# Kernel tuning notes

Measured on AMD Instinct MI355X. Metric: run time of the kernel, lower is better.

## Reference

```python
import jax, jax.numpy as jnp
import numpy as np

N = 8000      # nodes (spatial spots)
E = 40000     # directed edges (kNN graph, avg degree 5)
DIN = 1024    # input_dim
H = 3         # heads
C = 1024      # hidden_dim per head
NCLS = 460    # n_classes
NCEN = 100    # centroid count (pass-through only)
NEG_SLOPE = 0.2


def setup_inputs() -> dict:
    key = jax.random.key(0)
    ks = jax.random.split(key, 12)
    s_in = 1.0 / np.sqrt(DIN)   # glorot-ish scale for 1024 fan-in
    s_h = 1.0 / np.sqrt(C)
    return {
        'x': jax.random.normal(ks[0], (N, DIN), jnp.float32),
        'edge_index': jax.random.randint(ks[1], (E, 2), 0, N),  # [E,2] (src,dst)
        'Wl': jax.random.normal(ks[2], (DIN, H * C), jnp.float32) * s_in,
        'bl': jnp.zeros((H * C,), jnp.float32),
        'Wr': jax.random.normal(ks[3], (DIN, H * C), jnp.float32) * s_in,
        'br': jnp.zeros((H * C,), jnp.float32),
        'att': jax.random.normal(ks[4], (H, C), jnp.float32) * s_h,
        'bias': jnp.zeros((C,), jnp.float32),
        'Wf': jax.random.normal(ks[5], (C, NCLS), jnp.float32) * s_h,
        'bf': jnp.zeros((NCLS,), jnp.float32),
        'exps': jax.random.uniform(ks[6], (N, NCLS), jnp.float32),
        'exps_c': jax.random.uniform(ks[7], (NCEN, NCLS), jnp.float32),
    }


def reference(x, edge_index, Wl, bl, Wr, br, att, bias, Wf, bf, exps, exps_c):
    n = x.shape[0]
    h_, c_ = att.shape
    # PyG GATv2Conv default add_self_loops=True
    loops = jnp.arange(n)
    src = jnp.concatenate([edge_index[:, 0], loops])
    dst = jnp.concatenate([edge_index[:, 1], loops])
    # lin_l / lin_r projections -> [N,H,C]
    xl = (x @ Wl + bl).reshape(n, h_, c_)
    xr = (x @ Wr + br).reshape(n, h_, c_)
    # GATv2 edge scores: a^T LeakyReLU(x_l[src] + x_r[dst])  -> [Etot,H]
    s = jax.nn.leaky_relu(xl[src] + xr[dst], NEG_SLOPE)
    e = jnp.einsum('ehc,hc->eh', s, att)
    # segment softmax over incoming edges per dst node (PyG softmax: +1e-16)
    m = jax.lax.stop_gradient(jax.ops.segment_max(e, dst, num_segments=n))
    a = jnp.exp(e - m[dst])
    denom = jax.ops.segment_sum(a, dst, num_segments=n)
    alpha = a / (denom[dst] + 1e-16)
    # weighted scatter-add of source messages
    out = jax.ops.segment_sum(alpha[:, :, None] * xl[src], dst, num_segments=n)
    # concat=False -> mean over heads, then conv bias
    out = out.mean(axis=1) + bias
    # fc + row softmax
    h = jax.nn.softmax(out @ Wf + bf, axis=-1)
    return h
```

## Files before the change

kernel.cpp:

```cpp
#include <hip/hip_runtime.h>

#define NNODES 8000
#define MPAD   8064
#define NEDGES 40000
#define ETOT   (NEDGES + NNODES)
#define DIN    1024
#define NH     3
#define CH     1024
#define HC     (NH * CH)
#define NTOT   (2 * HC)
#define NCLS   460
#define NCLS_P 512
#define NEG    0.2f

typedef _Float16 h8 __attribute__((ext_vector_type(8)));
typedef _Float16 h4v __attribute__((ext_vector_type(4)));
typedef float    f4 __attribute__((ext_vector_type(4)));

__global__ __launch_bounds__(256)
void fp16_pad_convert(const float* __restrict__ in, _Float16* __restrict__ out,
                      int rows_in, int rows_out, int cols)
{
    size_t i4 = (size_t)blockIdx.x * 256 + threadIdx.x;
    size_t tot = ((size_t)rows_out * cols) >> 2;
    if (i4 >= tot) return;
    size_t e = i4 << 2;
    int row = (int)(e / cols);
    float vx = 0.f, vy = 0.f, vz = 0.f, vw = 0.f;
    if (row < rows_in) {
        float4 v = *(const float4*)(in + e);
        vx = v.x; vy = v.y; vz = v.z; vw = v.w;
    }
    h4v o = { (_Float16)vx, (_Float16)vy, (_Float16)vz, (_Float16)vw };
    *(h4v*)(out + e) = o;
}

__global__ __launch_bounds__(256)
void transpose_to_fp16(const float* __restrict__ W, _Float16* __restrict__ Wt,
                       int K, int Ncols, int rowOff)
{
    __shared__ float tile[32][33];
    int n0 = blockIdx.x * 32, k0 = blockIdx.y * 32;
    int tx = threadIdx.x, ty = threadIdx.y;
    #pragma unroll
    for (int i = 0; i < 4; ++i) {
        int k = k0 + ty + i * 8;
        int n = n0 + tx;
        tile[ty + i * 8][tx] = (n < Ncols) ? W[(size_t)k * Ncols + n] : 0.f;
    }
    __syncthreads();
    #pragma unroll
    for (int i = 0; i < 4; ++i) {
        int n = n0 + ty + i * 8;
        int k = k0 + tx;
        Wt[(size_t)(rowOff + n) * K + k] = (_Float16)tile[tx][ty + i * 8];
    }
}

__global__ __launch_bounds__(256)
void bias_pack(const float* __restrict__ bl, const float* __restrict__ br,
               const float* __restrict__ bf, float* __restrict__ b1, float* __restrict__ b2)
{
    int i = blockIdx.x * 256 + threadIdx.x;
    if (i < HC) { b1[i] = bl[i]; b1[HC + i] = br[i]; }
    if (i < NCLS_P) b2[i] = (i < NCLS) ? bf[i] : 0.f;
}

__global__ __launch_bounds__(256)
void csr_count(const int* __restrict__ ei, int* __restrict__ cnt)
{
    int e = blockIdx.x * 256 + threadIdx.x;
    if (e >= ETOT) return;
    int dst = (e < NEDGES) ? ei[2 * e + 1] : (e - NEDGES);
    atomicAdd(&cnt[dst], 1);
}

__global__ __launch_bounds__(1024)
void csr_scan(const int* __restrict__ cnt, int* __restrict__ rofs)
{
    __shared__ int s[1024];
    int t = threadIdx.x;
    int base = t * 8;
    int local[8];
    int sum = 0;
    #pragma unroll
    for (int i = 0; i < 8; ++i) {
        local[i] = sum;
        sum += (base + i < NNODES) ? cnt[base + i] : 0;
    }
    s[t] = sum;
    __syncthreads();
    for (int off = 1; off < 1024; off <<= 1) {
        int v = (t >= off) ? s[t - off] : 0;
        __syncthreads();
        if (t >= off) s[t] += v;
        __syncthreads();
    }
    int pre = (t > 0) ? s[t - 1] : 0;
    #pragma unroll
    for (int i = 0; i < 8; ++i)
        if (base + i < NNODES) rofs[base + i] = pre + local[i];
}

__global__ __launch_bounds__(256)
void csr_fill(const int* __restrict__ ei, const int* __restrict__ rofs,
              int* __restrict__ cursor, int* __restrict__ csr_src)
{
    int e = blockIdx.x * 256 + threadIdx.x;
    if (e >= ETOT) return;
    int src, dst;
    if (e < NEDGES) { src = ei[2 * e]; dst = ei[2 * e + 1]; }
    else            { src = dst = e - NEDGES; }
    int pos = rofs[dst] + atomicAdd(&cursor[dst], 1);
    csr_src[pos] = src;
}

__global__ __launch_bounds__(256, 3)
void gemm_f16(const _Float16* __restrict__ A, const _Float16* __restrict__ Bt,
              const float* __restrict__ biasN,
              float* __restrict__ C32, _Float16* __restrict__ C16,
              int N, int K)
{
    __shared__ __align__(16) _Float16 sA[128 * 32];
    __shared__ __align__(16) _Float16 sB[128 * 32];

    int nwg = gridDim.x;
    int orig = blockIdx.x;
    int q = nwg >> 3, r = nwg & 7;
    int xcd = orig & 7, idx = orig >> 3;
    int wg = (xcd < r ? xcd * (q + 1) : r * (q + 1) + (xcd - r) * q) + idx;
    int nbx = N >> 7;
    int bm = wg / nbx, bn = wg - bm * nbx;
    int m0 = bm << 7, n0 = bn << 7;

    const int t = threadIdx.x;
    const int lane = t & 63, w = t >> 6;
    const int wr = (w >> 1) << 6, wc = (w & 1) << 6;

    f4 acc[4][4];
    f4 zero = { 0.f, 0.f, 0.f, 0.f };
    #pragma unroll
    for (int i = 0; i < 4; ++i)
        #pragma unroll
        for (int j = 0; j < 4; ++j) acc[i][j] = zero;

    const int r0 = t >> 2, ks0 = t & 3;
    const int r1 = r0 + 64;
    const int wA0 = r0 * 32 + ((ks0 ^ ((r0 >> 1) & 3)) << 3);
    const int wA1 = r1 * 32 + ((ks0 ^ ((r1 >> 1) & 3)) << 3);
    const _Float16* gA0 = A  + (size_t)(m0 + r0) * K + ks0 * 8;
    const _Float16* gA1 = A  + (size_t)(m0 + r1) * K + ks0 * 8;
    const _Float16* gB0 = Bt + (size_t)(n0 + r0) * K + ks0 * 8;
    const _Float16* gB1 = Bt + (size_t)(n0 + r1) * K + ks0 * 8;

    uint4 stA0 = *(const uint4*)gA0;
    uint4 stA1 = *(const uint4*)gA1;
    uint4 stB0 = *(const uint4*)gB0;
    uint4 stB1 = *(const uint4*)gB1;

    const int nk = K >> 5;
    for (int s = 0; s < nk; ++s) {
        __syncthreads();
        *(uint4*)&sA[wA0] = stA0;
        *(uint4*)&sA[wA1] = stA1;
        *(uint4*)&sB[wA0] = stB0;
        *(uint4*)&sB[wA1] = stB1;
        __syncthreads();
        if (s + 1 < nk) {
            int koff = (s + 1) << 5;
            stA0 = *(const uint4*)(gA0 + koff);
            stA1 = *(const uint4*)(gA1 + koff);
            stB0 = *(const uint4*)(gB0 + koff);
            stB1 = *(const uint4*)(gB1 + koff);
        }
        const int ks = lane >> 4;
        h8 bh[4];
        #pragma unroll
        for (int nj = 0; nj < 4; ++nj) {
            int rn = wc + nj * 16 + (lane & 15);
            bh[nj] = *(const h8*)&sB[rn * 32 + ((ks ^ ((rn >> 1) & 3)) << 3)];
        }
        #pragma unroll
        for (int mi = 0; mi < 4; ++mi) {
            int rm = wr + mi * 16 + (lane & 15);
            h8 ah = *(const h8*)&sA[rm * 32 + ((ks ^ ((rm >> 1) & 3)) << 3)];
            #pragma unroll
            for (int nj = 0; nj < 4; ++nj)
                acc[mi][nj] = __builtin_amdgcn_mfma_f32_16x16x32_f16(ah, bh[nj], acc[mi][nj], 0, 0, 0);
        }
    }

    #pragma unroll
    for (int mi = 0; mi < 4; ++mi) {
        #pragma unroll
        for (int nj = 0; nj < 4; ++nj) {
            int col  = n0 + wc + nj * 16 + (lane & 15);
            int rowb = m0 + wr + mi * 16 + ((lane >> 4) << 2);
            float b = biasN[col];
            #pragma unroll
            for (int rg = 0; rg < 4; ++rg) {
                float v = acc[mi][nj][rg] + b;
                size_t off = (size_t)(rowb + rg) * N + col;
                if (C32) C32[off] = v;
                else     C16[off] = (_Float16)v;
            }
        }
    }
}

__global__ __launch_bounds__(384)
void edge_fused(const _Float16* __restrict__ xlr, const int* __restrict__ rofs,
                const int* __restrict__ cnt, const int* __restrict__ csr_src,
                const float* __restrict__ att, const float* __restrict__ bias,
                _Float16* __restrict__ o2h)
{
    __shared__ float red[6];
    __shared__ float outs[HC];

    const int dst = blockIdx.x;
    const int t   = threadIdx.x;
    const int h   = t >> 7;
    const int c0  = (t & 127) << 3;
    const int wid = t >> 6;

    h8 xrv = *(const h8*)(xlr + (size_t)dst * NTOT + HC + h * CH + c0);
    float xrf[8], atf[8];
    {
        float4 a0 = *(const float4*)(att + h * CH + c0);
        float4 a1 = *(const float4*)(att + h * CH + c0 + 4);
        atf[0] = a0.x; atf[1] = a0.y; atf[2] = a0.z; atf[3] = a0.w;
        atf[4] = a1.x; atf[5] = a1.y; atf[6] = a1.z; atf[7] = a1.w;
        #pragma unroll
        for (int j = 0; j < 8; ++j) xrf[j] = (float)xrv[j];
    }

    const int beg = rofs[dst];
    const int num = cnt[dst];

    float m = -3.4e38f, d = 0.f;
    float acc[8];
    #pragma unroll
    for (int j = 0; j < 8; ++j) acc[j] = 0.f;

    for (int i = 0; i < num; ++i) {
        int src = csr_src[beg + i];
        h8 xv = *(const h8*)(xlr + (size_t)src * NTOT + h * CH + c0);
        float s = 0.f;
        #pragma unroll
        for (int j = 0; j < 8; ++j) {
            float z = (float)xv[j] + xrf[j];
            z = z > 0.f ? z : NEG * z;
            s = fmaf(atf[j], z, s);
        }
        #pragma unroll
        for (int off = 32; off > 0; off >>= 1) s += __shfl_down(s, off);
        if ((t & 63) == 0) red[wid] = s;
        __syncthreads();
        float e = red[h << 1] + red[(h << 1) + 1];
        float nm = fmaxf(m, e);
        float sc_ = __expf(m - nm);
        float w   = __expf(e - nm);
        d = d * sc_ + w;
        #pragma unroll
        for (int j = 0; j < 8; ++j) acc[j] = fmaf(w, (float)xv[j], acc[j] * sc_);
        m = nm;
        __syncthreads();
    }

    float inv = 1.f / (d + 1e-16f) * (1.f / 3.f);
    #pragma unroll
    for (int j = 0; j < 8; ++j) outs[h * CH + c0 + j] = acc[j] * inv;
    __syncthreads();

    if (t < 256) {
        int c = t << 2;
        float4 b = *(const float4*)(bias + c);
        float v0 = outs[c + 0] + outs[CH + c + 0] + outs[2 * CH + c + 0] + b.x;
        float v1 = outs[c + 1] + outs[CH + c + 1] + outs[2 * CH + c + 1] + b.y;
        float v2 = outs[c + 2] + outs[CH + c + 2] + outs[2 * CH + c + 2] + b.z;
        float v3 = outs[c + 3] + outs[CH + c + 3] + outs[2 * CH + c + 3] + b.w;
        h4v o = { (_Float16)v0, (_Float16)v1, (_Float16)v2, (_Float16)v3 };
        *(h4v*)(o2h + (size_t)dst * CH + c) = o;
    }
}

__global__ __launch_bounds__(64)
void row_softmax(const float* __restrict__ logits, float* __restrict__ out)
{
    const int r = blockIdx.x;
    const int lane = threadIdx.x;
    const float* row = logits + (size_t)r * NCLS_P;
    float v[8];
    float mx = -3.4e38f;
    #pragma unroll
    for (int i = 0; i < 8; ++i) {
        int c = lane + i * 64;
        v[i] = (c < NCLS) ? row[c] : -3.4e38f;
        mx = fmaxf(mx, v[i]);
    }
    #pragma unroll
    for (int off = 32; off > 0; off >>= 1) mx = fmaxf(mx, __shfl_xor(mx, off));
    float s = 0.f;
    #pragma unroll
    for (int i = 0; i < 8; ++i) {
        int c = lane + i * 64;
        float ev = (c < NCLS) ? expf(v[i] - mx) : 0.f;
        v[i] = ev;
        s += ev;
    }
    #pragma unroll
    for (int off = 32; off > 0; off >>= 1) s += __shfl_xor(s, off);
    float inv = 1.f / s;
    #pragma unroll
    for (int i = 0; i < 8; ++i) {
        int c = lane + i * 64;
        if (c < NCLS) out[(size_t)r * NCLS + c] = v[i] * inv;
    }
}

extern "C" void kernel_launch(void* const* d_in, const int* in_sizes, int n_in,
                              void* d_out, int out_size, void* d_ws, size_t ws_size,
                              hipStream_t stream)
{
    (void)in_sizes; (void)n_in; (void)out_size; (void)ws_size;

    const float* x    = (const float*)d_in[0];
    const int*   ei   = (const int*)  d_in[1];
    const float* Wl   = (const float*)d_in[2];
    const float* bl   = (const float*)d_in[3];
    const float* Wr   = (const float*)d_in[4];
    const float* br   = (const float*)d_in[5];
    const float* att  = (const float*)d_in[6];
    const float* bias = (const float*)d_in[7];
    const float* Wf   = (const float*)d_in[8];
    const float* bf   = (const float*)d_in[9];

    char* base = (char*)d_ws;
    _Float16* xh      = (_Float16*)(base);
    _Float16* BtW     = (_Float16*)(base + 16515072);
    _Float16* Wft     = (_Float16*)(base + 29097984);
    float*    biasC1  = (float*)   (base + 30146560);
    float*    biasC2  = (float*)   (base + 30171136);
    int*      cnt     = (int*)     (base + 30173184);
    int*      cursor  = (int*)     (base + 30205184);
    int*      rofs    = (int*)     (base + 30237184);
    int*      csr_src = (int*)     (base + 30269184);
    _Float16* o2h     = (_Float16*)(base + 30461184);
    float*    logits  = (float*)   (base + 46976256);
    _Float16* xlr     = (_Float16*)(base + 63491328);

    hipMemsetAsync(cnt, 0, 64000, stream);
    hipMemsetAsync(o2h + (size_t)NNODES * CH, 0, (size_t)(MPAD - NNODES) * CH * 2, stream);

    fp16_pad_convert<<<(MPAD * DIN / 4 + 255) / 256, 256, 0, stream>>>(
        x, xh, NNODES, MPAD, DIN);

    transpose_to_fp16<<<dim3(HC / 32, DIN / 32), dim3(32, 8), 0, stream>>>(Wl, BtW, DIN, HC, 0);
    transpose_to_fp16<<<dim3(HC / 32, DIN / 32), dim3(32, 8), 0, stream>>>(Wr, BtW, DIN, HC, HC);
    transpose_to_fp16<<<dim3(NCLS_P / 32, DIN / 32), dim3(32, 8), 0, stream>>>(Wf, Wft, DIN, NCLS, 0);

    bias_pack<<<(HC + 255) / 256, 256, 0, stream>>>(bl, br, bf, biasC1, biasC2);

    csr_count<<<(ETOT + 255) / 256, 256, 0, stream>>>(ei, cnt);
    csr_scan<<<1, 1024, 0, stream>>>(cnt, rofs);
    csr_fill<<<(ETOT + 255) / 256, 256, 0, stream>>>(ei, rofs, cursor, csr_src);

    gemm_f16<<<(NTOT / 128) * (MPAD / 128), 256, 0, stream>>>(
        xh, BtW, biasC1, nullptr, xlr, NTOT, DIN);

    edge_fused<<<NNODES, 384, 0, stream>>>(xlr, rofs, cnt, csr_src, att, bias, o2h);

    gemm_f16<<<(NCLS_P / 128) * (MPAD / 128), 256, 0, stream>>>(
        o2h, Wft, biasC2, logits, nullptr, NCLS_P, DIN);

    row_softmax<<<NNODES, 64, 0, stream>>>(logits, (float*)d_out);
}
```

Measured before the change: 399.4 us.

## Use direct global-to-LDS loads in GEMM and one-wave-per-node edge kernel

```diff
diff --git a/kernel.cpp b/kernel.cpp
--- a/kernel.cpp
+++ b/kernel.cpp
@@ -17,6 +17,10 @@
 typedef _Float16 h4v __attribute__((ext_vector_type(4)));
 typedef float    f4 __attribute__((ext_vector_type(4)));
 
+#define GLOAD16(g, l) \
+    __builtin_amdgcn_global_load_lds((const __attribute__((address_space(1))) void*)(g), \
+                                     (__attribute__((address_space(3))) void*)(l), 16, 0, 0)
+
 __global__ __launch_bounds__(256)
 void fp16_pad_convert(const float* __restrict__ in, _Float16* __restrict__ out,
                       int rows_in, int rows_out, int cols)
@@ -59,10 +63,11 @@
 
 __global__ __launch_bounds__(256)
 void bias_pack(const float* __restrict__ bl, const float* __restrict__ br,
-               const float* __restrict__ bf, float* __restrict__ b1, float* __restrict__ b2)
+               const float* __restrict__ bf, const float* __restrict__ att,
+               float* __restrict__ b1, float* __restrict__ b2, _Float16* __restrict__ atth)
 {
     int i = blockIdx.x * 256 + threadIdx.x;
-    if (i < HC) { b1[i] = bl[i]; b1[HC + i] = br[i]; }
+    if (i < HC) { b1[i] = bl[i]; b1[HC + i] = br[i]; atth[i] = (_Float16)att[i]; }
     if (i < NCLS_P) b2[i] = (i < NCLS) ? bf[i] : 0.f;
 }
 
@@ -115,7 +120,7 @@
     csr_src[pos] = src;
 }
 
-__global__ __launch_bounds__(256, 3)
+__global__ __launch_bounds__(256, 4)
 void gemm_f16(const _Float16* __restrict__ A, const _Float16* __restrict__ Bt,
               const float* __restrict__ biasN,
               float* __restrict__ C32, _Float16* __restrict__ C16,
@@ -144,50 +149,36 @@
         #pragma unroll
         for (int j = 0; j < 4; ++j) acc[i][j] = zero;
 
-    const int r0 = t >> 2, ks0 = t & 3;
-    const int r1 = r0 + 64;
-    const int wA0 = r0 * 32 + ((ks0 ^ ((r0 >> 1) & 3)) << 3);
-    const int wA1 = r1 * 32 + ((ks0 ^ ((r1 >> 1) & 3)) << 3);
-    const _Float16* gA0 = A  + (size_t)(m0 + r0) * K + ks0 * 8;
-    const _Float16* gA1 = A  + (size_t)(m0 + r1) * K + ks0 * 8;
-    const _Float16* gB0 = Bt + (size_t)(n0 + r0) * K + ks0 * 8;
-    const _Float16* gB1 = Bt + (size_t)(n0 + r1) * K + ks0 * 8;
-
-    uint4 stA0 = *(const uint4*)gA0;
-    uint4 stA1 = *(const uint4*)gA1;
-    uint4 stB0 = *(const uint4*)gB0;
-    uint4 stB1 = *(const uint4*)gB1;
+    const int lr = lane >> 2, lk = lane & 3;
+    const _Float16* gA = A  + (size_t)(m0 + w * 16 + lr) * K + lk * 8;
+    const _Float16* gB = Bt + (size_t)(n0 + w * 16 + lr) * K + lk * 8;
+    _Float16* lA0 = &sA[w * 512];
+    _Float16* lA1 = &sA[2048 + w * 512];
+    _Float16* lB0 = &sB[w * 512];
+    _Float16* lB1 = &sB[2048 + w * 512];
+    const size_t seg = (size_t)64 * K;
 
     const int nk = K >> 5;
     for (int s = 0; s < nk; ++s) {
+        const int ko = s << 5;
+        GLOAD16(gA + ko,       lA0);
+        GLOAD16(gA + seg + ko, lA1);
+        GLOAD16(gB + ko,       lB0);
+        GLOAD16(gB + seg + ko, lB1);
         __syncthreads();
-        *(uint4*)&sA[wA0] = stA0;
-        *(uint4*)&sA[wA1] = stA1;
-        *(uint4*)&sB[wA0] = stB0;
-        *(uint4*)&sB[wA1] = stB1;
-        __syncthreads();
-        if (s + 1 < nk) {
-            int koff = (s + 1) << 5;
-            stA0 = *(const uint4*)(gA0 + koff);
-            stA1 = *(const uint4*)(gA1 + koff);
-            stB0 = *(const uint4*)(gB0 + koff);
-            stB1 = *(const uint4*)(gB1 + koff);
-        }
         const int ks = lane >> 4;
         h8 bh[4];
         #pragma unroll
-        for (int nj = 0; nj < 4; ++nj) {
-            int rn = wc + nj * 16 + (lane & 15);
-            bh[nj] = *(const h8*)&sB[rn * 32 + ((ks ^ ((rn >> 1) & 3)) << 3)];
-        }
+        for (int nj = 0; nj < 4; ++nj)
+            bh[nj] = *(const h8*)&sB[(wc + nj * 16 + (lane & 15)) * 32 + ks * 8];
         #pragma unroll
         for (int mi = 0; mi < 4; ++mi) {
-            int rm = wr + mi * 16 + (lane & 15);
-            h8 ah = *(const h8*)&sA[rm * 32 + ((ks ^ ((rm >> 1) & 3)) << 3)];
+            h8 ah = *(const h8*)&sA[(wr + mi * 16 + (lane & 15)) * 32 + ks * 8];
             #pragma unroll
             for (int nj = 0; nj < 4; ++nj)
                 acc[mi][nj] = __builtin_amdgcn_mfma_f32_16x16x32_f16(ah, bh[nj], acc[mi][nj], 0, 0, 0);
         }
+        __syncthreads();
     }
 
     #pragma unroll
@@ -208,79 +199,83 @@
     }
 }
 
-__global__ __launch_bounds__(384)
+__global__ __launch_bounds__(256)
 void edge_fused(const _Float16* __restrict__ xlr, const int* __restrict__ rofs,
                 const int* __restrict__ cnt, const int* __restrict__ csr_src,
-                const float* __restrict__ att, const float* __restrict__ bias,
+                const _Float16* __restrict__ atth, const float* __restrict__ bias,
                 _Float16* __restrict__ o2h)
 {
-    __shared__ float red[6];
-    __shared__ float outs[HC];
-
-    const int dst = blockIdx.x;
-    const int t   = threadIdx.x;
-    const int h   = t >> 7;
-    const int c0  = (t & 127) << 3;
-    const int wid = t >> 6;
-
-    h8 xrv = *(const h8*)(xlr + (size_t)dst * NTOT + HC + h * CH + c0);
-    float xrf[8], atf[8];
-    {
-        float4 a0 = *(const float4*)(att + h * CH + c0);
-        float4 a1 = *(const float4*)(att + h * CH + c0 + 4);
-        atf[0] = a0.x; atf[1] = a0.y; atf[2] = a0.z; atf[3] = a0.w;
-        atf[4] = a1.x; atf[5] = a1.y; atf[6] = a1.z; atf[7] = a1.w;
-        #pragma unroll
-        for (int j = 0; j < 8; ++j) xrf[j] = (float)xrv[j];
+    const int wid = threadIdx.x >> 6;
+    const int dst = (blockIdx.x << 2) + wid;
+    const int l   = threadIdx.x & 63;
+    const int cb0 = l << 3, cb1 = 512 + (l << 3);
+
+    h8 xr[3][2], at[3][2];
+    #pragma unroll
+    for (int h = 0; h < 3; ++h) {
+        const _Float16* pr = xlr + (size_t)dst * NTOT + HC + h * CH;
+        xr[h][0] = *(const h8*)(pr + cb0);
+        xr[h][1] = *(const h8*)(pr + cb1);
+        at[h][0] = *(const h8*)(atth + h * CH + cb0);
+        at[h][1] = *(const h8*)(atth + h * CH + cb1);
     }
 
     const int beg = rofs[dst];
     const int num = cnt[dst];
 
-    float m = -3.4e38f, d = 0.f;
-    float acc[8];
-    #pragma unroll
-    for (int j = 0; j < 8; ++j) acc[j] = 0.f;
+    float m[3] = { -3.4e38f, -3.4e38f, -3.4e38f };
+    float d[3] = { 0.f, 0.f, 0.f };
+    float acc[3][2][8] = {};
 
     for (int i = 0; i < num; ++i) {
         int src = csr_src[beg + i];
-        h8 xv = *(const h8*)(xlr + (size_t)src * NTOT + h * CH + c0);
-        float s = 0.f;
+        const _Float16* ps = xlr + (size_t)src * NTOT;
+        h8 xv[3][2];
+        #pragma unroll
+        for (int h = 0; h < 3; ++h) {
+            xv[h][0] = *(const h8*)(ps + h * CH + cb0);
+            xv[h][1] = *(const h8*)(ps + h * CH + cb1);
+        }
+        #pragma unroll
+        for (int h = 0; h < 3; ++h) {
+            float s = 0.f;
+            #pragma unroll
+            for (int b = 0; b < 2; ++b)
+                #pragma unroll
+                for (int j = 0; j < 8; ++j) {
+                    float z = (float)xv[h][b][j] + (float)xr[h][b][j];
+                    z = z > 0.f ? z : NEG * z;
+                    s = fmaf((float)at[h][b][j], z, s);
+                }
+            #pragma unroll
+            for (int off = 32; off > 0; off >>= 1) s += __shfl_xor(s, off);
+            float nm = fmaxf(m[h], s);
+            float rs = __expf(m[h] - nm);
+            float wt = __expf(s - nm);
+            d[h] = d[h] * rs + wt;
+            #pragma unroll
+            for (int b = 0; b < 2; ++b)
+                #pragma unroll
+                for (int j = 0; j < 8; ++j)
+                    acc[h][b][j] = fmaf(wt, (float)xv[h][b][j], acc[h][b][j] * rs);
+            m[h] = nm;
+        }
+    }
+
+    float inv0 = 1.f / (d[0] + 1e-16f) * (1.f / 3.f);
+    float inv1 = 1.f / (d[1] + 1e-16f) * (1.f / 3.f);
+    float inv2 = 1.f / (d[2] + 1e-16f) * (1.f / 3.f);
+    #pragma unroll
+    for (int b = 0; b < 2; ++b) {
+        int c = b ? cb1 : cb0;
+        h8 o;
         #pragma unroll
         for (int j = 0; j < 8; ++j) {
-            float z = (float)xv[j] + xrf[j];
-            z = z > 0.f ? z : NEG * z;
-            s = fmaf(atf[j], z, s);
-        }
-        #pragma unroll
-        for (int off = 32; off > 0; off >>= 1) s += __shfl_down(s, off);
-        if ((t & 63) == 0) red[wid] = s;
-        __syncthreads();
-        float e = red[h << 1] + red[(h << 1) + 1];
-        float nm = fmaxf(m, e);
-        float sc_ = __expf(m - nm);
-        float w   = __expf(e - nm);
-        d = d * sc_ + w;
-        #pragma unroll
-        for (int j = 0; j < 8; ++j) acc[j] = fmaf(w, (float)xv[j], acc[j] * sc_);
-        m = nm;
-        __syncthreads();
-    }
-
-    float inv = 1.f / (d + 1e-16f) * (1.f / 3.f);
-    #pragma unroll
-    for (int j = 0; j < 8; ++j) outs[h * CH + c0 + j] = acc[j] * inv;
-    __syncthreads();
-
-    if (t < 256) {
-        int c = t << 2;
-        float4 b = *(const float4*)(bias + c);
-        float v0 = outs[c + 0] + outs[CH + c + 0] + outs[2 * CH + c + 0] + b.x;
-        float v1 = outs[c + 1] + outs[CH + c + 1] + outs[2 * CH + c + 1] + b.y;
-        float v2 = outs[c + 2] + outs[CH + c + 2] + outs[2 * CH + c + 2] + b.z;
-        float v3 = outs[c + 3] + outs[CH + c + 3] + outs[2 * CH + c + 3] + b.w;
-        h4v o = { (_Float16)v0, (_Float16)v1, (_Float16)v2, (_Float16)v3 };
-        *(h4v*)(o2h + (size_t)dst * CH + c) = o;
+            float v = acc[0][b][j] * inv0 + acc[1][b][j] * inv1 + acc[2][b][j] * inv2
+                    + bias[c + j];
+            o[j] = (_Float16)v;
+        }
+        *(h8*)(o2h + (size_t)dst * CH + c) = o;
     }
 }
 
@@ -341,13 +336,14 @@
     _Float16* Wft     = (_Float16*)(base + 29097984);
     float*    biasC1  = (float*)   (base + 30146560);
     float*    biasC2  = (float*)   (base + 30171136);
-    int*      cnt     = (int*)     (base + 30173184);
-    int*      cursor  = (int*)     (base + 30205184);
-    int*      rofs    = (int*)     (base + 30237184);
-    int*      csr_src = (int*)     (base + 30269184);
-    _Float16* o2h     = (_Float16*)(base + 30461184);
-    float*    logits  = (float*)   (base + 46976256);
-    _Float16* xlr     = (_Float16*)(base + 63491328);
+    _Float16* atth    = (_Float16*)(base + 30173184);
+    int*      cnt     = (int*)     (base + 30179328);
+    int*      cursor  = (int*)     (base + 30211328);
+    int*      rofs    = (int*)     (base + 30243328);
+    int*      csr_src = (int*)     (base + 30275328);
+    _Float16* o2h     = (_Float16*)(base + 30467328);
+    float*    logits  = (float*)   (base + 46982400);
+    _Float16* xlr     = (_Float16*)(base + 63497472);
 
     hipMemsetAsync(cnt, 0, 64000, stream);
     hipMemsetAsync(o2h + (size_t)NNODES * CH, 0, (size_t)(MPAD - NNODES) * CH * 2, stream);
@@ -359,7 +355,7 @@
     transpose_to_fp16<<<dim3(HC / 32, DIN / 32), dim3(32, 8), 0, stream>>>(Wr, BtW, DIN, HC, HC);
     transpose_to_fp16<<<dim3(NCLS_P / 32, DIN / 32), dim3(32, 8), 0, stream>>>(Wf, Wft, DIN, NCLS, 0);
 
-    bias_pack<<<(HC + 255) / 256, 256, 0, stream>>>(bl, br, bf, biasC1, biasC2);
+    bias_pack<<<(HC + 255) / 256, 256, 0, stream>>>(bl, br, bf, att, biasC1, biasC2, atth);
 
     csr_count<<<(ETOT + 255) / 256, 256, 0, stream>>>(ei, cnt);
     csr_scan<<<1, 1024, 0, stream>>>(cnt, rofs);
@@ -368,7 +364,7 @@
     gemm_f16<<<(NTOT / 128) * (MPAD / 128), 256, 0, stream>>>(
         xh, BtW, biasC1, nullptr, xlr, NTOT, DIN);
 
-    edge_fused<<<NNODES, 384, 0, stream>>>(xlr, rofs, cnt, csr_src, att, bias, o2h);
+    edge_fused<<<NNODES / 4, 256, 0, stream>>>(xlr, rofs, cnt, csr_src, atth, bias, o2h);
 
     gemm_f16<<<(NCLS_P / 128) * (MPAD / 128), 256, 0, stream>>>(
         o2h, Wft, biasC2, logits, nullptr, NCLS_P, DIN);
```

Result: slower. 421.4 us (+5.5%).
